# Performance work log

Measured on AMD Instinct MI355X. Metric: run time of the kernel, lower is better.

Reference implementation:

```python
import jax, jax.numpy as jnp
import numpy as np

N = 100000
E = 3200000
F_IN = 128
H1, C1 = 2, 16          # conv1: heads=2, out_channels=16, concat -> 32
H2, C2 = 1, 40          # conv2: heads=1, out_channels=num_classes=40
NEG_SLOPE = 0.2


def setup_inputs() -> dict:
    key = jax.random.key(0)
    ks = jax.random.split(key, 12)
    features = jax.random.normal(ks[0], (N, F_IN), dtype=jnp.float32)
    edges = jax.random.randint(ks[1], (2, E), 0, N, dtype=jnp.int64)
    weight = jax.random.uniform(ks[2], (E,), dtype=jnp.float32)  # ignored (edge_dim=None)
    s = 0.1
    W1 = jax.random.normal(ks[3], (F_IN, H1 * C1), dtype=jnp.float32) * s
    att_src1 = jax.random.normal(ks[4], (H1, C1), dtype=jnp.float32) * s
    att_dst1 = jax.random.normal(ks[5], (H1, C1), dtype=jnp.float32) * s
    b1 = jnp.zeros((H1 * C1,), dtype=jnp.float32)
    W2 = jax.random.normal(ks[6], (H1 * C1, H2 * C2), dtype=jnp.float32) * s
    att_src2 = jax.random.normal(ks[7], (H2, C2), dtype=jnp.float32) * s
    att_dst2 = jax.random.normal(ks[8], (H2, C2), dtype=jnp.float32) * s
    b2 = jnp.zeros((H2 * C2,), dtype=jnp.float32)
    return {"features": features, "edges": edges, "weight": weight,
            "W1": W1, "att_src1": att_src1, "att_dst1": att_dst1, "b1": b1,
            "W2": W2, "att_src2": att_src2, "att_dst2": att_dst2, "b2": b2}


def _segment_softmax(e, seg, num_segments):
    # e: [E, H]; softmax over edges sharing the same destination node
    m = jax.ops.segment_max(e, seg, num_segments=num_segments)
    ex = jnp.exp(e - m[seg])
    s = jax.ops.segment_sum(ex, seg, num_segments=num_segments)
    return ex / (s[seg] + 1e-16)


def _gat_conv(x, src, dst, W, att_src, att_dst, bias, heads, out_ch):
    n = x.shape[0]
    h = (x @ W).reshape(n, heads, out_ch)                  # [N,H,C]
    a_src = jnp.sum(h * att_src, axis=-1)                  # [N,H]
    a_dst = jnp.sum(h * att_dst, axis=-1)                  # [N,H]
    e = a_src[src] + a_dst[dst]                            # [E,H]
    e = jnp.where(e > 0, e, NEG_SLOPE * e)                 # LeakyReLU(0.2)
    alpha = _segment_softmax(e, dst, n)                    # [E,H]
    msg = h[src] * alpha[:, :, None]                       # [E,H,C]
    out = jax.ops.segment_sum(msg, dst, num_segments=n)    # [N,H,C]
    return out.reshape(n, heads * out_ch) + bias           # concat=True


def reference(features, edges, weight, W1, att_src1, att_dst1, b1,
              W2, att_src2, att_dst2, b2):
    n = features.shape[0]
    # GATConv default add_self_loops=True (self-loop removal of pre-existing
    # loops skipped: negligible for random edges and not jit-shape-friendly)
    loop = jnp.arange(n, dtype=edges.dtype)
    src = jnp.concatenate([edges[0], loop])
    dst = jnp.concatenate([edges[1], loop])
    x = _gat_conv(features, src, dst, W1, att_src1, att_dst1, b1, H1, C1)
    x = jax.nn.relu(x)
    # F.dropout with training=self.training -> identity in eval mode
    x = _gat_conv(x, src, dst, W2, att_src2, att_dst2, b2, H2, C2)
    return x
```

## Files before the change

### kernel.cpp

```cpp
#include <hip/hip_runtime.h>


#define DEVFN __device__ __forceinline__
#define CB_SHIFT 8
#define CB_SZ 256
#define SC_CHUNK 4096
#define NBMAX 512
#define STASH 12288

DEVFN unsigned short f2h(float f) {
  _Float16 h = (_Float16)f;
  unsigned short u;
  __builtin_memcpy(&u, &h, 2);
  return u;
}
DEVFN float h2f(unsigned short u) {
  _Float16 h;
  __builtin_memcpy(&h, &u, 2);
  return (float)h;
}

DEVFN float lrelu(float e) { return e > 0.f ? e : 0.2f * e; }

DEVFN void acc8(float* acc, float x, uint4 u) {
  acc[0] = fmaf(x, h2f(u.x & 0xffff), acc[0]);
  acc[1] = fmaf(x, h2f(u.x >> 16),    acc[1]);
  acc[2] = fmaf(x, h2f(u.y & 0xffff), acc[2]);
  acc[3] = fmaf(x, h2f(u.y >> 16),    acc[3]);
  acc[4] = fmaf(x, h2f(u.z & 0xffff), acc[4]);
  acc[5] = fmaf(x, h2f(u.z >> 16),    acc[5]);
  acc[6] = fmaf(x, h2f(u.w & 0xffff), acc[6]);
  acc[7] = fmaf(x, h2f(u.w >> 16),    acc[7]);
}

DEVFN void read_edge(const long long* eg64, const int* eg32, int is64, int E,
                     int i, int& s, int& d) {
  if (i >= E) { s = d = i - E; return; }
  if (is64) { s = (int)eg64[i]; d = (int)eg64[E + i]; }
  else      { s = eg32[i];      d = eg32[E + i]; }
}

DEVFN int detect64(const int* eg32, int E, int i0, int t) {
  int base = i0;
  if (base > E - 64) base = E - 64;
  if (base < 0) base = 0;
  int i = base + (t & 63);
  unsigned long long m = __ballot((i < E) && (eg32[2 * i + 1] != 0));
  return m == 0ull;
}

__global__ __launch_bounds__(256) void bucket_hist(const long long* eg64,
                                                   const int* eg32,
                                                   int E, int N, int NB2,
                                                   int* __restrict__ bhist) {
  __shared__ int lh[NBMAX];
  int t = threadIdx.x;
  lh[t] = 0; lh[t + 256] = 0;
  int is64 = detect64(eg32, E, 0, t);
  __syncthreads();
  int EN = E + N;
  int step = (int)gridDim.x * 1024;
  for (int base = (int)blockIdx.x * 1024; base < EN; base += step) {
#pragma unroll
    for (int k = 0; k < 4; k++) {
      int i = base + k * 256 + t;
      if (i < EN) {
        int d;
        if (i >= E) d = i - E;
        else d = is64 ? (int)eg64[E + i] : eg32[E + i];
        atomicAdd(&lh[d >> CB_SHIFT], 1);
      }
    }
  }
  __syncthreads();
  if (t < NB2 && lh[t]) atomicAdd(&bhist[t], lh[t]);
  int t2 = t + 256;
  if (t2 < NB2 && lh[t2]) atomicAdd(&bhist[t2], lh[t2]);
}

__global__ void bucket_scan(const int* __restrict__ bhist,
                            int* __restrict__ bscan, int* __restrict__ gcur,
                            int NB2, int EN) {
  __shared__ int buf[2][NBMAX];
  int t = threadIdx.x;
  int v = (t < NB2) ? bhist[t] : 0;
  buf[0][t] = v;
  __syncthreads();
  int pin = 0;
  for (int off = 1; off < NBMAX; off <<= 1) {
    int nv = buf[pin][t] + (t >= off ? buf[pin][t - off] : 0);
    buf[1 - pin][t] = nv;
    pin ^= 1;
    __syncthreads();
  }
  int excl = buf[pin][t] - v;
  if (t < NB2) { bscan[t] = excl; gcur[t] = excl; }
  if (t == NB2) bscan[t] = EN;
}

__global__ __launch_bounds__(256) void chunk_scatter_sorted(
    const long long* eg64, const int* eg32, int E, int N, int NB2,
    int* __restrict__ gcur, int* __restrict__ tmp) {
  __shared__ int lh[NBMAX];
  __shared__ int lscan[NBMAX];
  __shared__ int lpos[NBMAX];
  __shared__ int gbase[NBMAX];
  __shared__ int sbuf[2][NBMAX];
  __shared__ int payl[SC_CHUNK];
  __shared__ unsigned short bktid[SC_CHUNK];
  int t = threadIdx.x;
  int i0 = (int)blockIdx.x * SC_CHUNK;
  int is64 = detect64(eg32, E, i0, t);
  lh[t] = 0; lh[t + 256] = 0;
  __syncthreads();
  int EN = E + N;
  int i1 = i0 + SC_CHUNK; if (i1 > EN) i1 = EN;
  int total = i1 - i0;
  int es[16], ed[16];
#pragma unroll
  for (int bb = 0; bb < 4; bb++) {
#pragma unroll
    for (int k = 0; k < 4; k++) {
      int idx = bb * 4 + k;
      int i = i0 + bb * 1024 + k * 256 + t;
      int s = 0, d = -1;
      if (i < i1) read_edge(eg64, eg32, is64, E, i, s, d);
      es[idx] = s; ed[idx] = d;
    }
  }
#pragma unroll
  for (int j = 0; j < 16; j++)
    if (ed[j] >= 0) atomicAdd(&lh[ed[j] >> CB_SHIFT], 1);
  __syncthreads();
  sbuf[0][t] = lh[t]; sbuf[0][t + 256] = lh[t + 256];
  __syncthreads();
  int pin = 0;
  for (int off = 1; off < NBMAX; off <<= 1) {
    int nv0 = sbuf[pin][t] + (t >= off ? sbuf[pin][t - off] : 0);
    int nv1 = sbuf[pin][t + 256] + sbuf[pin][t + 256 - off];
    __syncthreads();
    sbuf[1 - pin][t] = nv0; sbuf[1 - pin][t + 256] = nv1;
    pin ^= 1;
    __syncthreads();
  }
  lscan[t] = sbuf[pin][t] - lh[t];
  lscan[t + 256] = sbuf[pin][t + 256] - lh[t + 256];
  lpos[t] = lscan[t]; lpos[t + 256] = lscan[t + 256];
  if (t < NB2 && lh[t]) gbase[t] = atomicAdd(&gcur[t], lh[t]);
  int t2 = t + 256;
  if (t2 < NB2 && lh[t2]) gbase[t2] = atomicAdd(&gcur[t2], lh[t2]);
  __syncthreads();
#pragma unroll
  for (int j = 0; j < 16; j++) {
    if (ed[j] >= 0) {
      int b = ed[j] >> CB_SHIFT;
      int sl = atomicAdd(&lpos[b], 1);
      payl[sl] = (es[j] << CB_SHIFT) | (ed[j] & (CB_SZ - 1));
      bktid[sl] = (unsigned short)b;
    }
  }
  __syncthreads();
  for (int j = t; j < total; j += 256) {
    int b = bktid[j];
    tmp[gbase[b] + (j - lscan[b])] = payl[j];
  }
}

__global__ __launch_bounds__(256) void bucket_rp_sort(const int* __restrict__ bscan,
                                                      const int* __restrict__ tmp,
                                                      int* __restrict__ rp,
                                                      int* __restrict__ csr,
                                                      int N, int EN) {
  __shared__ int lc[CB_SZ];
  __shared__ int ps[256];
  __shared__ int lcur[CB_SZ];
  __shared__ int stash[STASH];
  int b = blockIdx.x, t = threadIdx.x;
  lc[t] = 0;
  __syncthreads();
  int w0 = bscan[b];
  int w1 = bscan[b + 1];
  int cnt = w1 - w0;
  bool fit = (cnt <= STASH);
  int p = w0 + t;
  for (; p + 768 < w1; p += 1024) {
    int e0 = tmp[p], e1 = tmp[p + 256], e2 = tmp[p + 512], e3 = tmp[p + 768];
    if (fit) {
      stash[p - w0] = e0; stash[p - w0 + 256] = e1;
      stash[p - w0 + 512] = e2; stash[p - w0 + 768] = e3;
    }
    atomicAdd(&lc[e0 & (CB_SZ - 1)], 1);
    atomicAdd(&lc[e1 & (CB_SZ - 1)], 1);
    atomicAdd(&lc[e2 & (CB_SZ - 1)], 1);
    atomicAdd(&lc[e3 & (CB_SZ - 1)], 1);
  }
  if (p < w1) {
    bool v1 = p + 256 < w1, v2 = p + 512 < w1;
    int q1 = v1 ? p + 256 : p;
    int q2 = v2 ? p + 512 : p;
    int e0 = tmp[p], e1 = tmp[q1], e2 = tmp[q2];
    if (fit) {
      stash[p - w0] = e0;
      if (v1) stash[q1 - w0] = e1;
      if (v2) stash[q2 - w0] = e2;
    }
    atomicAdd(&lc[e0 & (CB_SZ - 1)], 1);
    if (v1) atomicAdd(&lc[e1 & (CB_SZ - 1)], 1);
    if (v2) atomicAdd(&lc[e2 & (CB_SZ - 1)], 1);
  }
  __syncthreads();
  int a = lc[t];
  ps[t] = a;
  __syncthreads();
  for (int off = 1; off < 256; off <<= 1) {
    int v = ps[t];
    int u = (t >= off) ? ps[t - off] : 0;
    __syncthreads();
    ps[t] = v + u;
    __syncthreads();
  }
  int base = w0 + ps[t] - a;
  lcur[t] = base;
  int n0 = b * CB_SZ;
  if (n0 + t < N) rp[n0 + t] = base;
  if (b == (int)gridDim.x - 1 && t == 0) rp[N] = EN;
  __syncthreads();
  if (fit) {
    for (int j = t; j < cnt; j += 256) {
      int e = stash[j];
      int pos = atomicAdd(&lcur[e & (CB_SZ - 1)], 1);
      csr[pos] = e >> CB_SHIFT;
    }
  } else {
    for (int q = w0 + t; q < w1; q += 256) {
      int e = tmp[q];
      int pos = atomicAdd(&lcur[e & (CB_SZ - 1)], 1);
      csr[pos] = e >> CB_SHIFT;
    }
  }
}

__global__ __launch_bounds__(256) void gemm1f(const float* __restrict__ X,
                                              const float* __restrict__ W,
                                              const float* __restrict__ att_s,
                                              const float* __restrict__ att_d,
                                              uint4* __restrict__ h1h,
                                              float* __restrict__ as1,
                                              float* __restrict__ ad1, int N) {
  __shared__ float Wl[128 * 32];
  __shared__ float Asl[32], Adl[32];
  int t = threadIdx.x;
  for (int i = t; i < 1024; i += 256)
    ((float4*)Wl)[i] = ((const float4*)W)[i];
  if (t < 32) { Asl[t] = att_s[t]; Adl[t] = att_d[t]; }
  __syncthreads();
  int n = blockIdx.x * 256 + t;
  if (n >= N) return;
  const float4* X4 = (const float4*)(X + (size_t)n * 128);
  float acc[32];
#pragma unroll
  for (int c = 0; c < 32; c++) acc[c] = 0.f;
  for (int k4 = 0; k4 < 32; k4++) {
    float4 x = X4[k4];
    const float4* w4 = (const float4*)(Wl + k4 * 128);
#pragma unroll
    for (int c4 = 0; c4 < 8; c4++) {
      float4 w0 = w4[c4], w1 = w4[8 + c4], w2 = w4[16 + c4], w3 = w4[24 + c4];
      float* A = acc + c4 * 4;
      A[0] = fmaf(x.x, w0.x, A[0]); A[1] = fmaf(x.x, w0.y, A[1]);
      A[2] = fmaf(x.x, w0.z, A[2]); A[3] = fmaf(x.x, w0.w, A[3]);
      A[0] = fmaf(x.y, w1.x, A[0]); A[1] = fmaf(x.y, w1.y, A[1]);
      A[2] = fmaf(x.y, w1.z, A[2]); A[3] = fmaf(x.y, w1.w, A[3]);
      A[0] = fmaf(x.z, w2.x, A[0]); A[1] = fmaf(x.z, w2.y, A[1]);
      A[2] = fmaf(x.z, w2.z, A[2]); A[3] = fmaf(x.z, w2.w, A[3]);
      A[0] = fmaf(x.w, w3.x, A[0]); A[1] = fmaf(x.w, w3.y, A[1]);
      A[2] = fmaf(x.w, w3.z, A[2]); A[3] = fmaf(x.w, w3.w, A[3]);
    }
  }
  float s0 = 0.f, d0 = 0.f, s1 = 0.f, d1 = 0.f;
#pragma unroll
  for (int c = 0; c < 16; c++) {
    s0 = fmaf(acc[c], Asl[c], s0);
    d0 = fmaf(acc[c], Adl[c], d0);
    s1 = fmaf(acc[16 + c], Asl[16 + c], s1);
    d1 = fmaf(acc[16 + c], Adl[16 + c], d1);
  }
  as1[n * 2] = s0; as1[n * 2 + 1] = s1;
  ad1[n * 2] = d0; ad1[n * 2 + 1] = d1;
#pragma unroll
  for (int j = 0; j < 4; j++) {
    uint4 u;
    u.x = (unsigned)f2h(acc[j * 8 + 0]) | ((unsigned)f2h(acc[j * 8 + 1]) << 16);
    u.y = (unsigned)f2h(acc[j * 8 + 2]) | ((unsigned)f2h(acc[j * 8 + 3]) << 16);
    u.z = (unsigned)f2h(acc[j * 8 + 4]) | ((unsigned)f2h(acc[j * 8 + 5]) << 16);
    u.w = (unsigned)f2h(acc[j * 8 + 6]) | ((unsigned)f2h(acc[j * 8 + 7]) << 16);
    h1h[(size_t)n * 4 + j] = u;
  }
}

__global__ __launch_bounds__(256, 8) void agg1_attn(
    const int* __restrict__ rp, const int* __restrict__ csr,
    const float* __restrict__ as, const float* __restrict__ ad,
    const uint4* __restrict__ h1h, const float* __restrict__ b1,
    const float* __restrict__ W2, const float* __restrict__ as2w,
    const float* __restrict__ ad2w, uint4* __restrict__ x1h,
    float* __restrict__ as2, float* __restrict__ ad2, int N) {
  __shared__ float val[32], vbl[32];
  int t = threadIdx.x;
  if (t < 32) {
    float a = 0.f, b = 0.f;
    for (int c = 0; c < 40; c++) {
      float w = W2[t * 40 + c];
      a = fmaf(w, as2w[c], a);
      b = fmaf(w, ad2w[c], b);
    }
    val[t] = a; vbl[t] = b;
  }
  __syncthreads();
  int nl = t >> 4, r = t & 15;
  int half = r >> 2, cq = r & 3;
  int h = cq >> 1;
  int n = blockIdx.x * 16 + nl;
  float acc[8] = {0, 0, 0, 0, 0, 0, 0, 0};
  float ssum = 0.f;
  if (n < N) {
    int p0 = rp[n], p1 = rp[n + 1];
    float adv = ad[n * 2 + h];
    int p = p0 + half;
    for (; p + 12 < p1; p += 16) {
      int sA = csr[p], sB = csr[p + 4], sC = csr[p + 8], sD = csr[p + 12];
      float eA = as[sA * 2 + h] + adv;
      float eB = as[sB * 2 + h] + adv;
      float eC = as[sC * 2 + h] + adv;
      float eD = as[sD * 2 + h] + adv;
      uint4 uA = h1h[(size_t)sA * 4 + cq];
      uint4 uB = h1h[(size_t)sB * 4 + cq];
      uint4 uC = h1h[(size_t)sC * 4 + cq];
      uint4 uD = h1h[(size_t)sD * 4 + cq];
      float xA = __expf(lrelu(eA));
      float xB = __expf(lrelu(eB));
      float xC = __expf(lrelu(eC));
      float xD = __expf(lrelu(eD));
      ssum += (xA + xB) + (xC + xD);
      acc8(acc, xA, uA);
      acc8(acc, xB, uB);
      acc8(acc, xC, uC);
      acc8(acc, xD, uD);
    }
    if (p < p1) {
      bool vB = p + 4 < p1, vC = p + 8 < p1;
      int pB = vB ? p + 4 : p;
      int pC = vC ? p + 8 : p;
      int sA = csr[p], sB = csr[pB], sC = csr[pC];
      float eA = as[sA * 2 + h] + adv;
      float eB = as[sB * 2 + h] + adv;
      float eC = as[sC * 2 + h] + adv;
      uint4 uA = h1h[(size_t)sA * 4 + cq];
      uint4 uB = h1h[(size_t)sB * 4 + cq];
      uint4 uC = h1h[(size_t)sC * 4 + cq];
      float xA = __expf(lrelu(eA));
      float xB = vB ? __expf(lrelu(eB)) : 0.f;
      float xC = vC ? __expf(lrelu(eC)) : 0.f;
      ssum += xA + xB + xC;
      acc8(acc, xA, uA);
      acc8(acc, xB, uB);
      acc8(acc, xC, uC);
    }
  }
#pragma unroll
  for (int j = 0; j < 8; j++) acc[j] += __shfl_xor(acc[j], 4);
  ssum += __shfl_xor(ssum, 4);
#pragma unroll
  for (int j = 0; j < 8; j++) acc[j] += __shfl_xor(acc[j], 8);
  ssum += __shfl_xor(ssum, 8);
  if (n < N && half == 0) {
    float inv = 1.0f / (ssum + 1e-16f);
    float4 ba = ((const float4*)b1)[cq * 2];
    float4 bb = ((const float4*)b1)[cq * 2 + 1];
    float xv[8];
    xv[0] = fmaxf(fmaf(acc[0], inv, ba.x), 0.f);
    xv[1] = fmaxf(fmaf(acc[1], inv, ba.y), 0.f);
    xv[2] = fmaxf(fmaf(acc[2], inv, ba.z), 0.f);
    xv[3] = fmaxf(fmaf(acc[3], inv, ba.w), 0.f);
    xv[4] = fmaxf(fmaf(acc[4], inv, bb.x), 0.f);
    xv[5] = fmaxf(fmaf(acc[5], inv, bb.y), 0.f);
    xv[6] = fmaxf(fmaf(acc[6], inv, bb.z), 0.f);
    xv[7] = fmaxf(fmaf(acc[7], inv, bb.w), 0.f);
    uint4 u;
    u.x = (unsigned)f2h(xv[0]) | ((unsigned)f2h(xv[1]) << 16);
    u.y = (unsigned)f2h(xv[2]) | ((unsigned)f2h(xv[3]) << 16);
    u.z = (unsigned)f2h(xv[4]) | ((unsigned)f2h(xv[5]) << 16);
    u.w = (unsigned)f2h(xv[6]) | ((unsigned)f2h(xv[7]) << 16);
    x1h[(size_t)n * 4 + cq] = u;
    int ch0 = cq * 8;
    float ss = 0.f, sd = 0.f;
#pragma unroll
    for (int j = 0; j < 8; j++) {
      ss = fmaf(xv[j], val[ch0 + j], ss);
      sd = fmaf(xv[j], vbl[ch0 + j], sd);
    }
    ss += __shfl_xor(ss, 1); sd += __shfl_xor(sd, 1);
    ss += __shfl_xor(ss, 2); sd += __shfl_xor(sd, 2);
    if (cq == 0) { as2[n] = ss; ad2[n] = sd; }
  }
}

__global__ __launch_bounds__(256, 8) void agg2_gemm(
    const int* __restrict__ rp, const int* __restrict__ csr,
    const float* __restrict__ as, const float* __restrict__ ad,
    const uint4* __restrict__ x1h, const float* __restrict__ W2,
    const float* __restrict__ b2, float* __restrict__ outp, int N) {
  __shared__ float Wl[32 * 40];
  __shared__ float xt[16][33];
  __shared__ float hr[16][41];
  int t = threadIdx.x;
  for (int i = t; i < 320; i += 256)
    ((float4*)Wl)[i] = ((const float4*)W2)[i];
  int nl = t >> 4, r = t & 15;
  int half = r >> 2, cq = r & 3;
  int n = blockIdx.x * 16 + nl;
  float acc[8] = {0, 0, 0, 0, 0, 0, 0, 0};
  float ssum = 0.f;
  if (n < N) {
    int p0 = rp[n], p1 = rp[n + 1];
    float adv = ad[n];
    int p = p0 + half;
    for (; p + 12 < p1; p += 16) {
      int sA = csr[p], sB = csr[p + 4], sC = csr[p + 8], sD = csr[p + 12];
      float eA = as[sA] + adv;
      float eB = as[sB] + adv;
      float eC = as[sC] + adv;
      float eD = as[sD] + adv;
      uint4 uA = x1h[(size_t)sA * 4 + cq];
      uint4 uB = x1h[(size_t)sB * 4 + cq];
      uint4 uC = x1h[(size_t)sC * 4 + cq];
      uint4 uD = x1h[(size_t)sD * 4 + cq];
      float xA = __expf(lrelu(eA));
      float xB = __expf(lrelu(eB));
      float xC = __expf(lrelu(eC));
      float xD = __expf(lrelu(eD));
      ssum += (xA + xB) + (xC + xD);
      acc8(acc, xA, uA);
      acc8(acc, xB, uB);
      acc8(acc, xC, uC);
      acc8(acc, xD, uD);
    }
    if (p < p1) {
      bool vB = p + 4 < p1, vC = p + 8 < p1;
      int pB = vB ? p + 4 : p;
      int pC = vC ? p + 8 : p;
      int sA = csr[p], sB = csr[pB], sC = csr[pC];
      float eA = as[sA] + adv;
      float eB = as[sB] + adv;
      float eC = as[sC] + adv;
      uint4 uA = x1h[(size_t)sA * 4 + cq];
      uint4 uB = x1h[(size_t)sB * 4 + cq];
      uint4 uC = x1h[(size_t)sC * 4 + cq];
      float xA = __expf(lrelu(eA));
      float xB = vB ? __expf(lrelu(eB)) : 0.f;
      float xC = vC ? __expf(lrelu(eC)) : 0.f;
      ssum += xA + xB + xC;
      acc8(acc, xA, uA);
      acc8(acc, xB, uB);
      acc8(acc, xC, uC);
    }
  }
#pragma unroll
  for (int j = 0; j < 8; j++) acc[j] += __shfl_xor(acc[j], 4);
  ssum += __shfl_xor(ssum, 4);
#pragma unroll
  for (int j = 0; j < 8; j++) acc[j] += __shfl_xor(acc[j], 8);
  ssum += __shfl_xor(ssum, 8);
  if (n < N && half == 0) {
    float inv = 1.0f / (ssum + 1e-16f);
    int ch0 = cq * 8;
#pragma unroll
    for (int j = 0; j < 8; j++) xt[nl][ch0 + j] = acc[j] * inv;
  }
  __syncthreads();
  if (n < N && r < 8) {
    float a2[5] = {0, 0, 0, 0, 0};
    int cb = r * 5;
    for (int k = 0; k < 32; k++) {
      float x = xt[nl][k];
#pragma unroll
      for (int c = 0; c < 5; c++)
        a2[c] = fmaf(x, Wl[k * 40 + cb + c], a2[c]);
    }
#pragma unroll
    for (int c = 0; c < 5; c++) hr[nl][cb + c] = a2[c];
  }
  __syncthreads();
  if (n < N && r < 10) {
    const float* s = hr[nl] + r * 4;
    float4 bb = ((const float4*)b2)[r];
    float4 v;
    v.x = s[0] + bb.x; v.y = s[1] + bb.y;
    v.z = s[2] + bb.z; v.w = s[3] + bb.w;
    ((float4*)outp)[(size_t)n * 10 + r] = v;
  }
}

extern "C" void kernel_launch(void* const* d_in, const int* in_sizes, int n_in,
                              void* d_out, int out_size, void* d_ws, size_t ws_size,
                              hipStream_t stream) {
  const float* X    = (const float*)d_in[0];
  const long long* eg64 = (const long long*)d_in[1];
  const int* eg32   = (const int*)d_in[1];
  const float* W1   = (const float*)d_in[3];
  const float* as1w = (const float*)d_in[4];
  const float* ad1w = (const float*)d_in[5];
  const float* b1   = (const float*)d_in[6];
  const float* W2   = (const float*)d_in[7];
  const float* as2w = (const float*)d_in[8];
  const float* ad2w = (const float*)d_in[9];
  const float* b2   = (const float*)d_in[10];
  float* out = (float*)d_out;

  const int N  = in_sizes[0] / 128;
  const int E  = in_sizes[1] / 2;
  const int EN = E + N;
  const int NB2 = (N + CB_SZ - 1) / CB_SZ;
  const int NWG = (EN + SC_CHUNK - 1) / SC_CHUNK;

  char* wbase = (char*)d_ws;
  size_t off = 0;
  auto alloc = [&](size_t bytes) -> void* {
    void* p = wbase + off;
    off += (bytes + 255) & ~(size_t)255;
    return p;
  };

  uint4* h1h = (uint4*)alloc((size_t)N * 64);
  size_t usz = (size_t)EN * 4;
  if ((size_t)N * 64 > usz) usz = (size_t)N * 64;
  char* uni = (char*)alloc(usz);
  uint4* x1h = (uint4*)uni;
  int*   tmp = (int*)uni;
  float* as1 = (float*)alloc((size_t)N * 2 * 4);
  float* ad1 = (float*)alloc((size_t)N * 2 * 4);
  float* as2 = (float*)alloc((size_t)N * 4);
  float* ad2 = (float*)alloc((size_t)N * 4);
  int* rp     = (int*)alloc((size_t)(N + 1) * 4);
  int* bhist  = (int*)alloc(NBMAX * 4);
  int* bscan  = (int*)alloc((NBMAX + 1) * 4);
  int* gcur   = (int*)alloc(NBMAX * 4);
  int* csr    = (int*)alloc((size_t)EN * 4);
  (void)ws_size; (void)n_in; (void)out_size;

  const int gN = (N + 255) / 256;

  hipMemsetAsync(bhist, 0, NBMAX * 4, stream);
  bucket_hist<<<1024, 256, 0, stream>>>(eg64, eg32, E, N, NB2, bhist);
  bucket_scan<<<1, NBMAX, 0, stream>>>(bhist, bscan, gcur, NB2, EN);
  chunk_scatter_sorted<<<NWG, 256, 0, stream>>>(eg64, eg32, E, N, NB2, gcur, tmp);
  bucket_rp_sort<<<NB2, 256, 0, stream>>>(bscan, tmp, rp, csr, N, EN);

  gemm1f<<<gN, 256, 0, stream>>>(X, W1, as1w, ad1w, h1h, as1, ad1, N);
  agg1_attn<<<(N + 15) / 16, 256, 0, stream>>>(rp, csr, as1, ad1, h1h, b1,
                                               W2, as2w, ad2w, x1h, as2, ad2, N);
  agg2_gemm<<<(N + 15) / 16, 256, 0, stream>>>(rp, csr, as2, ad2, x1h,
                                               W2, b2, out, N);
}
```

Before: 323.3 us.

## Split feature gathers into two half-width passes to shrink random-access working set

Feature tables are split into two 16-channel halves, and each aggregation kernel runs twice, once per half. Each pass gathers from a 3.2 MB table instead of 6.4 MB, which is meant to keep the random gathers in cache. Partial results are combined by adding into as2/ad2 and into the output, and the second layer applies the partial W2 product per half. The cost is reading the CSR, the attention scalars and the exp computation twice, plus extra kernel launches and read-modify-write traffic on the outputs.

```diff
diff --git a/kernel.cpp b/kernel.cpp
--- a/kernel.cpp
+++ b/kernel.cpp
@@ -244,7 +244,8 @@
                                               const float* __restrict__ W,
                                               const float* __restrict__ att_s,
                                               const float* __restrict__ att_d,
-                                              uint4* __restrict__ h1h,
+                                              uint4* __restrict__ h1a,
+                                              uint4* __restrict__ h1b,
                                               float* __restrict__ as1,
                                               float* __restrict__ ad1, int N) {
   __shared__ float Wl[128 * 32];
@@ -294,17 +295,18 @@
     u.y = (unsigned)f2h(acc[j * 8 + 2]) | ((unsigned)f2h(acc[j * 8 + 3]) << 16);
     u.z = (unsigned)f2h(acc[j * 8 + 4]) | ((unsigned)f2h(acc[j * 8 + 5]) << 16);
     u.w = (unsigned)f2h(acc[j * 8 + 6]) | ((unsigned)f2h(acc[j * 8 + 7]) << 16);
-    h1h[(size_t)n * 4 + j] = u;
-  }
-}
-
-__global__ __launch_bounds__(256, 8) void agg1_attn(
+    if (j < 2) h1a[(size_t)n * 2 + j] = u;
+    else       h1b[(size_t)n * 2 + (j - 2)] = u;
+  }
+}
+
+__global__ __launch_bounds__(256, 8) void agg1_pass(
     const int* __restrict__ rp, const int* __restrict__ csr,
     const float* __restrict__ as, const float* __restrict__ ad,
-    const uint4* __restrict__ h1h, const float* __restrict__ b1,
+    const uint4* __restrict__ h1p, const float* __restrict__ b1,
     const float* __restrict__ W2, const float* __restrict__ as2w,
-    const float* __restrict__ ad2w, uint4* __restrict__ x1h,
-    float* __restrict__ as2, float* __restrict__ ad2, int N) {
+    const float* __restrict__ ad2w, uint4* __restrict__ x1p,
+    float* __restrict__ as2, float* __restrict__ ad2, int N, int h, int addf) {
   __shared__ float val[32], vbl[32];
   int t = threadIdx.x;
   if (t < 32) {
@@ -318,25 +320,24 @@
   }
   __syncthreads();
   int nl = t >> 4, r = t & 15;
-  int half = r >> 2, cq = r & 3;
-  int h = cq >> 1;
+  int split = r >> 1, cq2 = r & 1;
   int n = blockIdx.x * 16 + nl;
   float acc[8] = {0, 0, 0, 0, 0, 0, 0, 0};
   float ssum = 0.f;
   if (n < N) {
     int p0 = rp[n], p1 = rp[n + 1];
     float adv = ad[n * 2 + h];
-    int p = p0 + half;
-    for (; p + 12 < p1; p += 16) {
-      int sA = csr[p], sB = csr[p + 4], sC = csr[p + 8], sD = csr[p + 12];
+    int p = p0 + split;
+    for (; p + 24 < p1; p += 32) {
+      int sA = csr[p], sB = csr[p + 8], sC = csr[p + 16], sD = csr[p + 24];
       float eA = as[sA * 2 + h] + adv;
       float eB = as[sB * 2 + h] + adv;
       float eC = as[sC * 2 + h] + adv;
       float eD = as[sD * 2 + h] + adv;
-      uint4 uA = h1h[(size_t)sA * 4 + cq];
-      uint4 uB = h1h[(size_t)sB * 4 + cq];
-      uint4 uC = h1h[(size_t)sC * 4 + cq];
-      uint4 uD = h1h[(size_t)sD * 4 + cq];
+      uint4 uA = h1p[(size_t)sA * 2 + cq2];
+      uint4 uB = h1p[(size_t)sB * 2 + cq2];
+      uint4 uC = h1p[(size_t)sC * 2 + cq2];
+      uint4 uD = h1p[(size_t)sD * 2 + cq2];
       float xA = __expf(lrelu(eA));
       float xB = __expf(lrelu(eB));
       float xC = __expf(lrelu(eC));
@@ -348,16 +349,16 @@
       acc8(acc, xD, uD);
     }
     if (p < p1) {
-      bool vB = p + 4 < p1, vC = p + 8 < p1;
-      int pB = vB ? p + 4 : p;
-      int pC = vC ? p + 8 : p;
+      bool vB = p + 8 < p1, vC = p + 16 < p1;
+      int pB = vB ? p + 8 : p;
+      int pC = vC ? p + 16 : p;
       int sA = csr[p], sB = csr[pB], sC = csr[pC];
       float eA = as[sA * 2 + h] + adv;
       float eB = as[sB * 2 + h] + adv;
       float eC = as[sC * 2 + h] + adv;
-      uint4 uA = h1h[(size_t)sA * 4 + cq];
-      uint4 uB = h1h[(size_t)sB * 4 + cq];
-      uint4 uC = h1h[(size_t)sC * 4 + cq];
+      uint4 uA = h1p[(size_t)sA * 2 + cq2];
+      uint4 uB = h1p[(size_t)sB * 2 + cq2];
+      uint4 uC = h1p[(size_t)sC * 2 + cq2];
       float xA = __expf(lrelu(eA));
       float xB = vB ? __expf(lrelu(eB)) : 0.f;
       float xC = vC ? __expf(lrelu(eC)) : 0.f;
@@ -368,15 +369,19 @@
     }
   }
 #pragma unroll
+  for (int j = 0; j < 8; j++) acc[j] += __shfl_xor(acc[j], 2);
+  ssum += __shfl_xor(ssum, 2);
+#pragma unroll
   for (int j = 0; j < 8; j++) acc[j] += __shfl_xor(acc[j], 4);
   ssum += __shfl_xor(ssum, 4);
 #pragma unroll
   for (int j = 0; j < 8; j++) acc[j] += __shfl_xor(acc[j], 8);
   ssum += __shfl_xor(ssum, 8);
-  if (n < N && half == 0) {
+  if (n < N && split == 0) {
     float inv = 1.0f / (ssum + 1e-16f);
-    float4 ba = ((const float4*)b1)[cq * 2];
-    float4 bb = ((const float4*)b1)[cq * 2 + 1];
+    int ch0 = h * 16 + cq2 * 8;
+    float4 ba = ((const float4*)b1)[ch0 >> 2];
+    float4 bb = ((const float4*)b1)[(ch0 >> 2) + 1];
     float xv[8];
     xv[0] = fmaxf(fmaf(acc[0], inv, ba.x), 0.f);
     xv[1] = fmaxf(fmaf(acc[1], inv, ba.y), 0.f);
@@ -391,8 +396,7 @@
     u.y = (unsigned)f2h(xv[2]) | ((unsigned)f2h(xv[3]) << 16);
     u.z = (unsigned)f2h(xv[4]) | ((unsigned)f2h(xv[5]) << 16);
     u.w = (unsigned)f2h(xv[6]) | ((unsigned)f2h(xv[7]) << 16);
-    x1h[(size_t)n * 4 + cq] = u;
-    int ch0 = cq * 8;
+    x1p[(size_t)n * 2 + cq2] = u;
     float ss = 0.f, sd = 0.f;
 #pragma unroll
     for (int j = 0; j < 8; j++) {
@@ -400,41 +404,43 @@
       sd = fmaf(xv[j], vbl[ch0 + j], sd);
     }
     ss += __shfl_xor(ss, 1); sd += __shfl_xor(sd, 1);
-    ss += __shfl_xor(ss, 2); sd += __shfl_xor(sd, 2);
-    if (cq == 0) { as2[n] = ss; ad2[n] = sd; }
-  }
-}
-
-__global__ __launch_bounds__(256, 8) void agg2_gemm(
+    if (cq2 == 0) {
+      if (addf) { as2[n] += ss; ad2[n] += sd; }
+      else      { as2[n] = ss;  ad2[n] = sd; }
+    }
+  }
+}
+
+__global__ __launch_bounds__(256, 8) void agg2_pass(
     const int* __restrict__ rp, const int* __restrict__ csr,
     const float* __restrict__ as, const float* __restrict__ ad,
-    const uint4* __restrict__ x1h, const float* __restrict__ W2,
-    const float* __restrict__ b2, float* __restrict__ outp, int N) {
-  __shared__ float Wl[32 * 40];
-  __shared__ float xt[16][33];
+    const uint4* __restrict__ x1p, const float* __restrict__ W2,
+    const float* __restrict__ b2, float* __restrict__ outp, int N, int k) {
+  __shared__ float Wl[16 * 40];
+  __shared__ float xt[16][17];
   __shared__ float hr[16][41];
   int t = threadIdx.x;
-  for (int i = t; i < 320; i += 256)
-    ((float4*)Wl)[i] = ((const float4*)W2)[i];
+  for (int i = t; i < 160; i += 256)
+    ((float4*)Wl)[i] = ((const float4*)(W2 + k * 640))[i];
   int nl = t >> 4, r = t & 15;
-  int half = r >> 2, cq = r & 3;
+  int split = r >> 1, cq2 = r & 1;
   int n = blockIdx.x * 16 + nl;
   float acc[8] = {0, 0, 0, 0, 0, 0, 0, 0};
   float ssum = 0.f;
   if (n < N) {
     int p0 = rp[n], p1 = rp[n + 1];
     float adv = ad[n];
-    int p = p0 + half;
-    for (; p + 12 < p1; p += 16) {
-      int sA = csr[p], sB = csr[p + 4], sC = csr[p + 8], sD = csr[p + 12];
+    int p = p0 + split;
+    for (; p + 24 < p1; p += 32) {
+      int sA = csr[p], sB = csr[p + 8], sC = csr[p + 16], sD = csr[p + 24];
       float eA = as[sA] + adv;
       float eB = as[sB] + adv;
       float eC = as[sC] + adv;
       float eD = as[sD] + adv;
-      uint4 uA = x1h[(size_t)sA * 4 + cq];
-      uint4 uB = x1h[(size_t)sB * 4 + cq];
-      uint4 uC = x1h[(size_t)sC * 4 + cq];
-      uint4 uD = x1h[(size_t)sD * 4 + cq];
+      uint4 uA = x1p[(size_t)sA * 2 + cq2];
+      uint4 uB = x1p[(size_t)sB * 2 + cq2];
+      uint4 uC = x1p[(size_t)sC * 2 + cq2];
+      uint4 uD = x1p[(size_t)sD * 2 + cq2];
       float xA = __expf(lrelu(eA));
       float xB = __expf(lrelu(eB));
       float xC = __expf(lrelu(eC));
@@ -446,16 +452,16 @@
       acc8(acc, xD, uD);
     }
     if (p < p1) {
-      bool vB = p + 4 < p1, vC = p + 8 < p1;
-      int pB = vB ? p + 4 : p;
-      int pC = vC ? p + 8 : p;
+      bool vB = p + 8 < p1, vC = p + 16 < p1;
+      int pB = vB ? p + 8 : p;
+      int pC = vC ? p + 16 : p;
       int sA = csr[p], sB = csr[pB], sC = csr[pC];
       float eA = as[sA] + adv;
       float eB = as[sB] + adv;
       float eC = as[sC] + adv;
-      uint4 uA = x1h[(size_t)sA * 4 + cq];
-      uint4 uB = x1h[(size_t)sB * 4 + cq];
-      uint4 uC = x1h[(size_t)sC * 4 + cq];
+      uint4 uA = x1p[(size_t)sA * 2 + cq2];
+      uint4 uB = x1p[(size_t)sB * 2 + cq2];
+      uint4 uC = x1p[(size_t)sC * 2 + cq2];
       float xA = __expf(lrelu(eA));
       float xB = vB ? __expf(lrelu(eB)) : 0.f;
       float xC = vC ? __expf(lrelu(eC)) : 0.f;
@@ -466,26 +472,28 @@
     }
   }
 #pragma unroll
+  for (int j = 0; j < 8; j++) acc[j] += __shfl_xor(acc[j], 2);
+  ssum += __shfl_xor(ssum, 2);
+#pragma unroll
   for (int j = 0; j < 8; j++) acc[j] += __shfl_xor(acc[j], 4);
   ssum += __shfl_xor(ssum, 4);
 #pragma unroll
   for (int j = 0; j < 8; j++) acc[j] += __shfl_xor(acc[j], 8);
   ssum += __shfl_xor(ssum, 8);
-  if (n < N && half == 0) {
+  if (n < N && split == 0) {
     float inv = 1.0f / (ssum + 1e-16f);
-    int ch0 = cq * 8;
-#pragma unroll
-    for (int j = 0; j < 8; j++) xt[nl][ch0 + j] = acc[j] * inv;
+#pragma unroll
+    for (int j = 0; j < 8; j++) xt[nl][cq2 * 8 + j] = acc[j] * inv;
   }
   __syncthreads();
   if (n < N && r < 8) {
     float a2[5] = {0, 0, 0, 0, 0};
     int cb = r * 5;
-    for (int k = 0; k < 32; k++) {
-      float x = xt[nl][k];
+    for (int k2 = 0; k2 < 16; k2++) {
+      float x = xt[nl][k2];
 #pragma unroll
       for (int c = 0; c < 5; c++)
-        a2[c] = fmaf(x, Wl[k * 40 + cb + c], a2[c]);
+        a2[c] = fmaf(x, Wl[k2 * 40 + cb + c], a2[c]);
     }
 #pragma unroll
     for (int c = 0; c < 5; c++) hr[nl][cb + c] = a2[c];
@@ -493,10 +501,16 @@
   __syncthreads();
   if (n < N && r < 10) {
     const float* s = hr[nl] + r * 4;
-    float4 bb = ((const float4*)b2)[r];
     float4 v;
-    v.x = s[0] + bb.x; v.y = s[1] + bb.y;
-    v.z = s[2] + bb.z; v.w = s[3] + bb.w;
+    if (k == 0) {
+      float4 bb = ((const float4*)b2)[r];
+      v.x = s[0] + bb.x; v.y = s[1] + bb.y;
+      v.z = s[2] + bb.z; v.w = s[3] + bb.w;
+    } else {
+      float4 o = ((const float4*)outp)[(size_t)n * 10 + r];
+      v.x = s[0] + o.x; v.y = s[1] + o.y;
+      v.z = s[2] + o.z; v.w = s[3] + o.w;
+    }
     ((float4*)outp)[(size_t)n * 10 + r] = v;
   }
 }
@@ -531,11 +545,13 @@
     return p;
   };
 
-  uint4* h1h = (uint4*)alloc((size_t)N * 64);
+  uint4* h1a = (uint4*)alloc((size_t)N * 32);
+  uint4* h1b = (uint4*)alloc((size_t)N * 32);
   size_t usz = (size_t)EN * 4;
   if ((size_t)N * 64 > usz) usz = (size_t)N * 64;
   char* uni = (char*)alloc(usz);
-  uint4* x1h = (uint4*)uni;
+  uint4* x1a = (uint4*)uni;
+  uint4* x1b = (uint4*)(uni + (size_t)N * 32);
   int*   tmp = (int*)uni;
   float* as1 = (float*)alloc((size_t)N * 2 * 4);
   float* ad1 = (float*)alloc((size_t)N * 2 * 4);
@@ -549,6 +565,7 @@
   (void)ws_size; (void)n_in; (void)out_size;
 
   const int gN = (N + 255) / 256;
+  const int gA = (N + 15) / 16;
 
   hipMemsetAsync(bhist, 0, NBMAX * 4, stream);
   bucket_hist<<<1024, 256, 0, stream>>>(eg64, eg32, E, N, NB2, bhist);
@@ -556,9 +573,11 @@
   chunk_scatter_sorted<<<NWG, 256, 0, stream>>>(eg64, eg32, E, N, NB2, gcur, tmp);
   bucket_rp_sort<<<NB2, 256, 0, stream>>>(bscan, tmp, rp, csr, N, EN);
 
-  gemm1f<<<gN, 256, 0, stream>>>(X, W1, as1w, ad1w, h1h, as1, ad1, N);
-  agg1_attn<<<(N + 15) / 16, 256, 0, stream>>>(rp, csr, as1, ad1, h1h, b1,
-                                               W2, as2w, ad2w, x1h, as2, ad2, N);
-  agg2_gemm<<<(N + 15) / 16, 256, 0, stream>>>(rp, csr, as2, ad2, x1h,
-                                               W2, b2, out, N);
-}
+  gemm1f<<<gN, 256, 0, stream>>>(X, W1, as1w, ad1w, h1a, h1b, as1, ad1, N);
+  agg1_pass<<<gA, 256, 0, stream>>>(rp, csr, as1, ad1, h1a, b1, W2, as2w,
+                                    ad2w, x1a, as2, ad2, N, 0, 0);
+  agg1_pass<<<gA, 256, 0, stream>>>(rp, csr, as1, ad1, h1b, b1, W2, as2w,
+                                    ad2w, x1b, as2, ad2, N, 1, 1);
+  agg2_pass<<<gA, 256, 0, stream>>>(rp, csr, as2, ad2, x1a, W2, b2, out, N, 0);
+  agg2_pass<<<gA, 256, 0, stream>>>(rp, csr, as2, ad2, x1b, W2, b2, out, N, 1);
+}
```

Result: slower. 390.6 us (+20.8%).
